# Optimization experiments

Hardware: AMD Instinct MI355X
Metric: run time of the kernel (lower is better)

The kernel has to match this reference:

```python
import jax, jax.numpy as jnp
import numpy as np

D = 1024
H = 16
HD = D // H


def setup_inputs() -> dict:
    key = jax.random.key(0)
    ks = jax.random.split(key, 13)
    s = 0.02
    inp = {
        "x": jax.random.normal(ks[0], (2, 2048, D), dtype=jnp.float32),
        "Wq": jax.random.normal(ks[1], (D, D), dtype=jnp.float32) * s,
        "bq": jnp.zeros((D,), jnp.float32),
        "Wk": jax.random.normal(ks[2], (D, D), dtype=jnp.float32) * s,
        "bk": jnp.zeros((D,), jnp.float32),
        "Wv": jax.random.normal(ks[3], (D, D), dtype=jnp.float32) * s,
        "bv": jnp.zeros((D,), jnp.float32),
        "Wo": jax.random.normal(ks[4], (D, D), dtype=jnp.float32) * s,
        "bo": jnp.zeros((D,), jnp.float32),
        "W1": jax.random.normal(ks[5], (D, 4 * D), dtype=jnp.float32) * s,
        "b1": jnp.zeros((4 * D,), jnp.float32),
        "W2": jax.random.normal(ks[6], (4 * D, D), dtype=jnp.float32) * s,
        "b2": jnp.zeros((D,), jnp.float32),
    }
    return inp


def reference(x, Wq, bq, Wk, bk, Wv, bv, Wo, bo, W1, b1, W2, b2):
    B, L, _ = x.shape
    # attention (dropout = identity in eval); note: original forward never applies norm1/norm2
    q = (x @ Wq + bq).reshape(B, L, H, HD).transpose(0, 2, 1, 3)  # [B,H,L,HD]
    k = (x @ Wk + bk).reshape(B, L, H, HD).transpose(0, 2, 1, 3)
    v = (x @ Wv + bv).reshape(B, L, H, HD).transpose(0, 2, 1, 3)
    s = jnp.einsum("bhqd,bhkd->bhqk", q, k) / jnp.sqrt(jnp.float32(HD))
    causal = jnp.tril(jnp.ones((L, L), dtype=bool))
    s = jnp.where(causal[None, None, :, :], s, -jnp.inf)
    p = jax.nn.softmax(s, axis=-1)
    y = jnp.einsum("bhqk,bhkd->bhqd", p, v)
    y = y.transpose(0, 2, 1, 3).reshape(B, L, D)
    x = x + (y @ Wo + bo)
    # MLP with SiLU
    h = jax.nn.silu(x @ W1 + b1)
    x = x + (h @ W2 + b2)
    return x
```

## Files before the change

kernel.cpp:

```cpp
#include <hip/hip_runtime.h>
#include <hip/hip_bf16.h>
#include <stdint.h>

using u16 = unsigned short;
typedef __bf16 bf16x8 __attribute__((ext_vector_type(8)));
typedef float f32x4 __attribute__((ext_vector_type(4)));
typedef u16 u16x8 __attribute__((ext_vector_type(8)));

__device__ __forceinline__ float bf2f(u16 u) {
  union { unsigned int i; float f; } v; v.i = ((unsigned int)u) << 16; return v.f;
}
__device__ __forceinline__ u16 f2bf(float f) {
  __bf16 h = (__bf16)f;
  return __builtin_bit_cast(u16, h);
}
__device__ __forceinline__ float fexp2(float x) {
  return __builtin_amdgcn_exp2f(x);
}

__device__ __forceinline__ void gload_lds16(const void* g, void* l) {
  __builtin_amdgcn_global_load_lds(
      (__attribute__((address_space(1))) const void*)g,
      (__attribute__((address_space(3))) void*)l, 16, 0, 0);
}

__global__ void cvt_f32_bf16(const float* __restrict__ in, u16* __restrict__ out) {
  int i = (blockIdx.x * 256 + threadIdx.x) * 8;
  float4 a = *(const float4*)(in + i);
  float4 b = *(const float4*)(in + i + 4);
  u16x8 o;
  o[0] = f2bf(a.x); o[1] = f2bf(a.y); o[2] = f2bf(a.z); o[3] = f2bf(a.w);
  o[4] = f2bf(b.x); o[5] = f2bf(b.y); o[6] = f2bf(b.z); o[7] = f2bf(b.w);
  *(u16x8*)(out + i) = o;
}

__global__ void transpose_cvt(const float* __restrict__ W, u16* __restrict__ Wt,
                              int K, int N) {
  __shared__ float t[32][33];
  const int tx = threadIdx.x & 31, ty = threadIdx.x >> 5;
  const int n0 = blockIdx.x * 32, k0 = blockIdx.y * 32;
#pragma unroll
  for (int i = 0; i < 32; i += 8)
    t[ty + i][tx] = W[(size_t)(k0 + ty + i) * N + n0 + tx];
  __syncthreads();
#pragma unroll
  for (int i = 0; i < 32; i += 8)
    Wt[(size_t)(n0 + ty + i) * K + k0 + tx] = f2bf(t[tx][ty + i]);
}

__global__ void transpose_cvt4(const float* __restrict__ Wa, const float* __restrict__ Wb,
                               const float* __restrict__ Wc, const float* __restrict__ Wd,
                               u16* __restrict__ Da, u16* __restrict__ Db,
                               u16* __restrict__ Dc, u16* __restrict__ Dd) {
  __shared__ float t[32][33];
  const int z = blockIdx.z;
  const float* W = (z == 0) ? Wa : (z == 1) ? Wb : (z == 2) ? Wc : Wd;
  u16* D = (z == 0) ? Da : (z == 1) ? Db : (z == 2) ? Dc : Dd;
  const int tx = threadIdx.x & 31, ty = threadIdx.x >> 5;
  const int n0 = blockIdx.x * 32, k0 = blockIdx.y * 32;
#pragma unroll
  for (int i = 0; i < 32; i += 8)
    t[ty + i][tx] = W[(size_t)(k0 + ty + i) * 1024 + n0 + tx];
  __syncthreads();
#pragma unroll
  for (int i = 0; i < 32; i += 8)
    D[(size_t)(n0 + ty + i) * 1024 + k0 + tx] = f2bf(t[tx][ty + i]);
}

__global__ void transpose_v(const u16* __restrict__ qkv, u16* __restrict__ vt) {
  __shared__ u16 tile[32][34];
  const int tx = threadIdx.x & 31, ty = threadIdx.x >> 5;
  const int kv0 = blockIdx.x * 32, d0 = blockIdx.y * 32;
  const int bh = blockIdx.z, b = bh >> 4, h = bh & 15;
#pragma unroll
  for (int i = 0; i < 32; i += 8)
    tile[ty + i][tx] = qkv[(size_t)(b * 2048 + kv0 + ty + i) * 3072 + 2048 + h * 64 + d0 + tx];
  __syncthreads();
#pragma unroll
  for (int i = 0; i < 32; i += 8)
    vt[((size_t)bh * 64 + d0 + ty + i) * 2048 + kv0 + tx] = tile[tx][ty + i];
}

__global__ void concat_bias(const float* __restrict__ bq, const float* __restrict__ bk,
                            const float* __restrict__ bv, float* __restrict__ o) {
  int i = blockIdx.x * 256 + threadIdx.x;
  o[i] = (i < 1024) ? bq[i] : (i < 2048 ? bk[i - 1024] : bv[i - 2048]);
}

template <int EPI>
__global__ __launch_bounds__(512, 2) void gemm256_kernel(
    const u16* __restrict__ A, const u16* __restrict__ Bt,
    const float* __restrict__ bias, u16* __restrict__ outb,
    int M, int N, int K) {
  __shared__ u16 As[4][8192];
  __shared__ u16 Bs[4][8192];
  const int t = threadIdx.x;
  const int w = t >> 6, lane = t & 63, lr = lane & 15, lg = lane >> 4;
  const int wm = w >> 2, wn = w & 3;
  const int gx = gridDim.x;
  const int nwg = gx * gridDim.y;
  const int p = blockIdx.y * gx + blockIdx.x;
  const int L = (p & 7) * (nwg >> 3) + (p >> 3);
  const int m0 = (L / gx) * 256, n0 = (L % gx) * 256;

  f32x4 acc[8][4] = {};
  bf16x8 bfr[4];
  const int NKT = K >> 5;

  auto stageA = [&](int kt) {
#pragma unroll
    for (int l = 0; l < 2; ++l) {
      int slot = l * 512 + t;
      int row = slot >> 2, cs = slot & 3;
      gload_lds16(&A[(size_t)(m0 + row) * K + kt * 32 + cs * 8], &As[kt & 3][slot * 8]);
    }
  };
  auto stageB = [&](int kt) {
#pragma unroll
    for (int l = 0; l < 2; ++l) {
      int slot = l * 512 + t;
      int row = slot >> 2, cs = slot & 3;
      gload_lds16(&Bt[(size_t)(n0 + row) * K + kt * 32 + cs * 8], &Bs[kt & 3][slot * 8]);
    }
  };

  stageA(0); stageB(0); stageA(1); stageB(1); stageA(2); stageB(2);
  asm volatile("s_waitcnt vmcnt(8)" ::: "memory");
  __builtin_amdgcn_s_barrier();

#define PHASE(Q, STAGE)                                                          \
  {                                                                              \
    const u16* Ab = &As[kt & 3][0];                                              \
    bf16x8 af[4];                                                                \
    _Pragma("unroll") for (int m = 0; m < 4; ++m)                                \
        af[m] = *(const bf16x8*)&Ab[(wm * 128 + ((Q) * 4 + m) * 16 + lr) * 32 +  \
                                    lg * 8];                                     \
    if ((Q) == 0) {                                                              \
      const u16* Bb = &Bs[kt & 3][0];                                            \
      _Pragma("unroll") for (int n = 0; n < 4; ++n)                              \
          bfr[n] = *(const bf16x8*)&Bb[(wn * 64 + n * 16 + lr) * 32 + lg * 8];   \
    }                                                                            \
    STAGE;                                                                       \
    __builtin_amdgcn_s_barrier();                                                \
    asm volatile("s_waitcnt lgkmcnt(0)" ::: "memory");                           \
    __builtin_amdgcn_sched_barrier(0);                                           \
    __builtin_amdgcn_s_setprio(1);                                               \
    _Pragma("unroll") for (int m = 0; m < 4; ++m)                                \
        _Pragma("unroll") for (int n = 0; n < 4; ++n)                            \
            acc[(Q) * 4 + m][n] = __builtin_amdgcn_mfma_f32_16x16x32_bf16(       \
                af[m], bfr[n], acc[(Q) * 4 + m][n], 0, 0, 0);                    \
    __builtin_amdgcn_s_setprio(0);                                               \
  }

  int kt = 0;
  for (; kt < NKT - 3; ++kt) {
    PHASE(0, stageA(kt + 3));
    __builtin_amdgcn_s_barrier();
    PHASE(1, stageB(kt + 3));
    asm volatile("s_waitcnt vmcnt(8)" ::: "memory");
    __builtin_amdgcn_s_barrier();
  }
  asm volatile("s_waitcnt vmcnt(0)" ::: "memory");
  __builtin_amdgcn_s_barrier();
  for (; kt < NKT; ++kt) {
    PHASE(0, (void)0);
    __builtin_amdgcn_s_barrier();
    PHASE(1, (void)0);
    __builtin_amdgcn_s_barrier();
  }
#undef PHASE

#pragma unroll
  for (int mf = 0; mf < 8; ++mf)
#pragma unroll
    for (int nf = 0; nf < 4; ++nf)
#pragma unroll
      for (int i = 0; i < 4; ++i) {
        int gr = m0 + wm * 128 + mf * 16 + lg * 4 + i;
        int gc = n0 + wn * 64 + nf * 16 + lr;
        float v = acc[mf][nf][i] + bias[gc];
        if constexpr (EPI == 1) v = v / (1.f + __expf(-v));
        outb[(size_t)gr * N + gc] = f2bf(v);
      }
}

template <int EPI>
__global__ __launch_bounds__(256) void gemm_nk64_kernel(
    const u16* __restrict__ A, const u16* __restrict__ Bt,
    const float* __restrict__ bias, const float* __restrict__ resid,
    u16* __restrict__ outb, float* __restrict__ outf, int M, int N, int K) {
  __shared__ u16 As[2][128 * 64];
  __shared__ u16 Bs[2][64 * 64];
  const int t = threadIdx.x;
  const int w = t >> 6, lane = t & 63, lr = lane & 15, lg = lane >> 4;
  const int wm = w >> 1, wn = w & 1;
  const int gx = gridDim.x;
  const int nwg = gx * gridDim.y;
  const int p = blockIdx.y * gx + blockIdx.x;
  const int L = (p & 7) * (nwg >> 3) + (p >> 3);
  const int m0 = (L / gx) * 128, n0 = (L % gx) * 64;

  f32x4 acc[4][2] = {};
  const int nt = K >> 6;

  auto stage = [&](int kt, int buf) {
#pragma unroll
    for (int it = 0; it < 4; ++it) {
      int ofs = (it * 256 + t) * 8;
      int row = ofs >> 6, slot = (ofs >> 3) & 7, ss = slot ^ (row & 7);
      gload_lds16(&A[(size_t)(m0 + row) * K + kt * 64 + ss * 8], &As[buf][ofs]);
    }
#pragma unroll
    for (int it = 0; it < 2; ++it) {
      int ofs = (it * 256 + t) * 8;
      int row = ofs >> 6, slot = (ofs >> 3) & 7, ss = slot ^ (row & 7);
      gload_lds16(&Bt[(size_t)(n0 + row) * K + kt * 64 + ss * 8], &Bs[buf][ofs]);
    }
  };

  stage(0, 0);
  __syncthreads();

  for (int kt = 0; kt < nt; ++kt) {
    const int cur = kt & 1;
    if (kt + 1 < nt) stage(kt + 1, cur ^ 1);
#pragma unroll
    for (int kk = 0; kk < 64; kk += 32) {
      const int kcol = kk + lg * 8;
      bf16x8 af[4], bfr[2];
#pragma unroll
      for (int m = 0; m < 4; ++m) {
        int row = wm * 64 + m * 16 + lr;
        int ss = (kcol >> 3) ^ (row & 7);
        af[m] = *(const bf16x8*)&As[cur][row * 64 + ss * 8];
      }
#pragma unroll
      for (int n = 0; n < 2; ++n) {
        int row = wn * 32 + n * 16 + lr;
        int ss = (kcol >> 3) ^ (row & 7);
        bfr[n] = *(const bf16x8*)&Bs[cur][row * 64 + ss * 8];
      }
#pragma unroll
      for (int m = 0; m < 4; ++m)
#pragma unroll
        for (int n = 0; n < 2; ++n)
          acc[m][n] = __builtin_amdgcn_mfma_f32_16x16x32_bf16(af[m], bfr[n],
                                                              acc[m][n], 0, 0, 0);
    }
    __syncthreads();
  }

  const int r0 = m0 + wm * 64, c0 = n0 + wn * 32;
#pragma unroll
  for (int m = 0; m < 4; ++m)
#pragma unroll
    for (int n = 0; n < 2; ++n)
#pragma unroll
      for (int i = 0; i < 4; ++i) {
        int gr = r0 + m * 16 + lg * 4 + i;
        int gc = c0 + n * 16 + lr;
        float v = acc[m][n][i] + bias[gc];
        if constexpr (EPI == 2 || EPI == 3) v += resid[(size_t)gr * N + gc];
        if constexpr (EPI == 2) {
          outf[(size_t)gr * N + gc] = v;
          outb[(size_t)gr * N + gc] = f2bf(v);
        }
        if constexpr (EPI == 3) outf[(size_t)gr * N + gc] = v;
      }
}

__global__ __launch_bounds__(256) void attn_kernel(const u16* __restrict__ qkv,
                                                   const u16* __restrict__ vtg,
                                                   u16* __restrict__ out) {
  __shared__ u16 Ks[2][64 * 64];
  __shared__ u16 Vs[2][64 * 64];
  __shared__ u16 Ps[4][16 * 64];
  const int t = threadIdx.x, w = t >> 6, lane = t & 63, lr = lane & 15, lg = lane >> 4;
  const int p = blockIdx.y * 32 + blockIdx.x;
  const int L = (p & 7) * 128 + (p >> 3);
  const int qt = 31 - (L & 31), bh = L >> 5, b = bh >> 4, h = bh & 15;
  const int qbw = qt * 64 + w * 16;

  const float QS = 0.18033688011f;
  bf16x8 qf[2];
#pragma unroll
  for (int kc = 0; kc < 2; ++kc) {
    const u16x8 v = *(const u16x8*)&qkv[(size_t)(b * 2048 + qbw + lr) * 3072 +
                                        h * 64 + kc * 32 + lg * 8];
    bf16x8 q;
#pragma unroll
    for (int jj = 0; jj < 8; ++jj) q[jj] = (__bf16)(bf2f(v[jj]) * QS);
    qf[kc] = q;
  }

  f32x4 yacc[4] = {};
  float S = 0.f;

  auto stage = [&](int j, int buf) {
#pragma unroll
    for (int it = 0; it < 2; ++it) {
      int ofs = (it * 256 + t) * 8;
      int row = ofs >> 6, slot = (ofs >> 3) & 7, ss = slot ^ (row & 7);
      gload_lds16(&qkv[(size_t)(b * 2048 + j * 64 + row) * 3072 + 1024 + h * 64 + ss * 8],
                  &Ks[buf][ofs]);
      gload_lds16(&vtg[((size_t)bh * 64 + row) * 2048 + j * 64 + ss * 8],
                  &Vs[buf][ofs]);
    }
  };

  stage(0, 0);
  __syncthreads();

  for (int j = 0; j <= qt; ++j) {
    const int cur = j & 1;
    if (j < qt) stage(j + 1, cur ^ 1);

    bf16x8 kf[2][4];
#pragma unroll
    for (int kc = 0; kc < 2; ++kc)
#pragma unroll
      for (int n = 0; n < 4; ++n) {
        int row = n * 16 + lr;
        kf[kc][n] = *(const bf16x8*)((const char*)&Ks[cur][0] + row * 128 +
                                     ((kc * 64 + lg * 16) ^ ((row & 7) << 4)));
      }
    f32x4 s[4] = {};
#pragma unroll
    for (int n = 0; n < 4; ++n)
#pragma unroll
      for (int kc = 0; kc < 2; ++kc)
        s[n] = __builtin_amdgcn_mfma_f32_16x16x32_bf16(kf[kc][n], qf[kc],
                                                       s[n], 0, 0, 0);
    if (j == qt) {
#pragma unroll
      for (int n = 0; n < 4; ++n)
#pragma unroll
        for (int i = 0; i < 4; ++i) {
          int kabs = j * 64 + n * 16 + lg * 4 + i;
          int qabs = qbw + lr;
          if (kabs > qabs) s[n][i] = -1e30f;
        }
    }
    {
      float rs = 0.f;
#pragma unroll
      for (int n = 0; n < 4; ++n)
#pragma unroll
        for (int i = 0; i < 4; ++i) {
          float pv = fexp2(s[n][i]);
          s[n][i] = pv;
          rs += pv;
        }
      S += rs;
      const int qrow = lr, sw = (qrow & 7) << 4;
#pragma unroll
      for (int n = 0; n < 4; ++n) {
        ushort4 ph;
        ph.x = f2bf(s[n][0]); ph.y = f2bf(s[n][1]);
        ph.z = f2bf(s[n][2]); ph.w = f2bf(s[n][3]);
        *(ushort4*)((char*)&Ps[w][0] + qrow * 128 + ((n * 32 + lg * 8) ^ sw)) = ph;
      }
    }
#pragma unroll
    for (int kc = 0; kc < 2; ++kc) {
      bf16x8 pa, vtf[4];
      {
        int qrow = lr;
        pa = *(const bf16x8*)((const char*)&Ps[w][0] + qrow * 128 +
                              ((kc * 64 + lg * 16) ^ ((qrow & 7) << 4)));
      }
#pragma unroll
      for (int n = 0; n < 4; ++n) {
        int row = n * 16 + lr;
        vtf[n] = *(const bf16x8*)((const char*)&Vs[cur][0] + row * 128 +
                                  ((kc * 64 + lg * 16) ^ ((row & 7) << 4)));
      }
#pragma unroll
      for (int n = 0; n < 4; ++n)
        yacc[n] = __builtin_amdgcn_mfma_f32_16x16x32_bf16(pa, vtf[n],
                                                          yacc[n], 0, 0, 0);
    }
    __syncthreads();
  }

  {
    float Sv = S;
    Sv += __shfl_xor(Sv, 16, 64);
    Sv += __shfl_xor(Sv, 32, 64);
    float inv = 1.f / Sv;
#pragma unroll
    for (int i = 0; i < 4; ++i) {
      float ivq = __shfl(inv, lg * 4 + i, 64);
#pragma unroll
      for (int n = 0; n < 4; ++n) {
        int row = b * 2048 + qbw + lg * 4 + i;
        int col = h * 64 + n * 16 + lr;
        out[(size_t)row * 1024 + col] = f2bf(yacc[n][i] * ivq);
      }
    }
  }
}

extern "C" void kernel_launch(void* const* d_in, const int* in_sizes, int n_in,
                              void* d_out, int out_size, void* d_ws, size_t ws_size,
                              hipStream_t stream) {
  const float* x  = (const float*)d_in[0];
  const float* Wq = (const float*)d_in[1];
  const float* bq = (const float*)d_in[2];
  const float* Wk = (const float*)d_in[3];
  const float* bk = (const float*)d_in[4];
  const float* Wv = (const float*)d_in[5];
  const float* bv = (const float*)d_in[6];
  const float* Wo = (const float*)d_in[7];
  const float* bo = (const float*)d_in[8];
  const float* W1 = (const float*)d_in[9];
  const float* b1 = (const float*)d_in[10];
  const float* W2 = (const float*)d_in[11];
  const float* b2 = (const float*)d_in[12];
  float* out = (float*)d_out;

  char* ws = (char*)d_ws;
  const size_t MB = 1u << 20;
  u16*   xb    = (u16*)(ws + 0);
  u16*   wtqkv = (u16*)(ws + 8 * MB);
  u16*   wto   = (u16*)(ws + 14 * MB);
  u16*   wt1   = (u16*)(ws + 16 * MB);
  u16*   wt2   = (u16*)(ws + 24 * MB);
  float* bqkv  = (float*)(ws + 32 * MB);
  u16*   qkv   = (u16*)(ws + 33 * MB);
  u16*   attn  = (u16*)(ws + 57 * MB);
  float* x2f   = (float*)(ws + 65 * MB);
  u16*   x2b   = (u16*)(ws + 81 * MB);
  u16*   hbuf  = (u16*)(ws + 89 * MB);
  u16*   vtg   = xb;

  cvt_f32_bf16<<<2048, 256, 0, stream>>>(x, xb);
  transpose_cvt4<<<dim3(32, 32, 4), 256, 0, stream>>>(
      Wq, Wk, Wv, Wo, wtqkv, wtqkv + 1024 * 1024, wtqkv + 2 * 1024 * 1024, wto);
  transpose_cvt<<<dim3(128, 32), 256, 0, stream>>>(W1, wt1, 1024, 4096);
  transpose_cvt<<<dim3(32, 128), 256, 0, stream>>>(W2, wt2, 4096, 1024);
  concat_bias<<<12, 256, 0, stream>>>(bq, bk, bv, bqkv);

  gemm256_kernel<0><<<dim3(12, 16), 512, 0, stream>>>(
      xb, wtqkv, bqkv, qkv, 4096, 3072, 1024);
  transpose_v<<<dim3(64, 2, 32), 256, 0, stream>>>(qkv, vtg);
  attn_kernel<<<dim3(32, 32), 256, 0, stream>>>(qkv, vtg, attn);
  gemm_nk64_kernel<2><<<dim3(16, 32), 256, 0, stream>>>(
      attn, wto, bo, x, x2b, x2f, 4096, 1024, 1024);
  gemm256_kernel<1><<<dim3(16, 16), 512, 0, stream>>>(
      x2b, wt1, b1, hbuf, 4096, 4096, 1024);
  gemm_nk64_kernel<3><<<dim3(16, 32), 256, 0, stream>>>(
      hbuf, wt2, b2, x2f, nullptr, out, 4096, 1024, 4096);
}
```

Baseline: 236.3 us.

## Split-K the W2 GEMM with atomic accumulation into pre-initialized output

```diff
diff --git a/kernel.cpp b/kernel.cpp
--- a/kernel.cpp
+++ b/kernel.cpp
@@ -184,11 +184,11 @@
       }
 }
 
-template <int EPI>
 __global__ __launch_bounds__(256) void gemm_nk64_kernel(
     const u16* __restrict__ A, const u16* __restrict__ Bt,
     const float* __restrict__ bias, const float* __restrict__ resid,
-    u16* __restrict__ outb, float* __restrict__ outf, int M, int N, int K) {
+    u16* __restrict__ outb, const float* __restrict__ bias2,
+    float* __restrict__ outinit, int M, int N, int K) {
   __shared__ u16 As[2][128 * 64];
   __shared__ u16 Bs[2][64 * 64];
   const int t = threadIdx.x;
@@ -259,13 +259,83 @@
       for (int i = 0; i < 4; ++i) {
         int gr = r0 + m * 16 + lg * 4 + i;
         int gc = c0 + n * 16 + lr;
-        float v = acc[m][n][i] + bias[gc];
-        if constexpr (EPI == 2 || EPI == 3) v += resid[(size_t)gr * N + gc];
-        if constexpr (EPI == 2) {
-          outf[(size_t)gr * N + gc] = v;
-          outb[(size_t)gr * N + gc] = f2bf(v);
-        }
-        if constexpr (EPI == 3) outf[(size_t)gr * N + gc] = v;
+        float v = acc[m][n][i] + bias[gc] + resid[(size_t)gr * N + gc];
+        outb[(size_t)gr * N + gc] = f2bf(v);
+        outinit[(size_t)gr * N + gc] = v + bias2[gc];
+      }
+}
+
+__global__ __launch_bounds__(256) void gemm_splitk_atomic(
+    const u16* __restrict__ A, const u16* __restrict__ Bt,
+    float* __restrict__ out, int M, int N, int K) {
+  __shared__ u16 As[2][128 * 64];
+  __shared__ u16 Bs[2][128 * 64];
+  const int t = threadIdx.x;
+  const int w = t >> 6, lane = t & 63, lr = lane & 15, lg = lane >> 4;
+  const int wm = w >> 1, wn = w & 1;
+  const int gx = gridDim.x;
+  const int nwg = gx * gridDim.y;
+  const int p = blockIdx.y * gx + blockIdx.x;
+  const int L = (p & 7) * (nwg >> 3) + (p >> 3);
+  const int m0 = (L / gx) * 128, n0 = (L % gx) * 128;
+  const int KH = K >> 1;
+  const int kbase = blockIdx.z * KH;
+
+  f32x4 acc[4][4] = {};
+  const int nt = KH >> 6;
+
+  auto stage = [&](int kt, int buf) {
+#pragma unroll
+    for (int it = 0; it < 4; ++it) {
+      int ofs = (it * 256 + t) * 8;
+      int row = ofs >> 6, slot = (ofs >> 3) & 7, ss = slot ^ (row & 7);
+      gload_lds16(&A[(size_t)(m0 + row) * K + kbase + kt * 64 + ss * 8], &As[buf][ofs]);
+      gload_lds16(&Bt[(size_t)(n0 + row) * K + kbase + kt * 64 + ss * 8], &Bs[buf][ofs]);
+    }
+  };
+
+  stage(0, 0);
+  __syncthreads();
+
+  for (int kt = 0; kt < nt; ++kt) {
+    const int cur = kt & 1;
+    if (kt + 1 < nt) stage(kt + 1, cur ^ 1);
+#pragma unroll
+    for (int kk = 0; kk < 64; kk += 32) {
+      const int kcol = kk + lg * 8;
+      bf16x8 af[4], bfr[4];
+#pragma unroll
+      for (int m = 0; m < 4; ++m) {
+        int row = wm * 64 + m * 16 + lr;
+        int ss = (kcol >> 3) ^ (row & 7);
+        af[m] = *(const bf16x8*)&As[cur][row * 64 + ss * 8];
+      }
+#pragma unroll
+      for (int n = 0; n < 4; ++n) {
+        int row = wn * 64 + n * 16 + lr;
+        int ss = (kcol >> 3) ^ (row & 7);
+        bfr[n] = *(const bf16x8*)&Bs[cur][row * 64 + ss * 8];
+      }
+#pragma unroll
+      for (int m = 0; m < 4; ++m)
+#pragma unroll
+        for (int n = 0; n < 4; ++n)
+          acc[m][n] = __builtin_amdgcn_mfma_f32_16x16x32_bf16(af[m], bfr[n],
+                                                              acc[m][n], 0, 0, 0);
+    }
+    __syncthreads();
+  }
+
+  const int r0 = m0 + wm * 64, c0 = n0 + wn * 64;
+#pragma unroll
+  for (int m = 0; m < 4; ++m)
+#pragma unroll
+    for (int n = 0; n < 4; ++n)
+#pragma unroll
+      for (int i = 0; i < 4; ++i) {
+        int gr = r0 + m * 16 + lg * 4 + i;
+        int gc = c0 + n * 16 + lr;
+        atomicAdd(&out[(size_t)gr * N + gc], acc[m][n][i]);
       }
 }
 
@@ -429,7 +499,6 @@
   float* bqkv  = (float*)(ws + 32 * MB);
   u16*   qkv   = (u16*)(ws + 33 * MB);
   u16*   attn  = (u16*)(ws + 57 * MB);
-  float* x2f   = (float*)(ws + 65 * MB);
   u16*   x2b   = (u16*)(ws + 81 * MB);
   u16*   hbuf  = (u16*)(ws + 89 * MB);
   u16*   vtg   = xb;
@@ -445,10 +514,10 @@
       xb, wtqkv, bqkv, qkv, 4096, 3072, 1024);
   transpose_v<<<dim3(64, 2, 32), 256, 0, stream>>>(qkv, vtg);
   attn_kernel<<<dim3(32, 32), 256, 0, stream>>>(qkv, vtg, attn);
-  gemm_nk64_kernel<2><<<dim3(16, 32), 256, 0, stream>>>(
-      attn, wto, bo, x, x2b, x2f, 4096, 1024, 1024);
+  gemm_nk64_kernel<<<dim3(16, 32), 256, 0, stream>>>(
+      attn, wto, bo, x, x2b, b2, out, 4096, 1024, 1024);
   gemm256_kernel<1><<<dim3(16, 16), 512, 0, stream>>>(
       x2b, wt1, b1, hbuf, 4096, 4096, 1024);
-  gemm_nk64_kernel<3><<<dim3(16, 32), 256, 0, stream>>>(
-      hbuf, wt2, b2, x2f, nullptr, out, 4096, 1024, 4096);
-}
+  gemm_splitk_atomic<<<dim3(8, 32, 2), 256, 0, stream>>>(
+      hbuf, wt2, out, 4096, 1024, 4096);
+}
```

After: 239.7 us. Within noise of the previous version (+1.4%).
